# Performance work log

Hardware: AMD Instinct MI355X
Metric: run time of the kernel (lower is better)

Reference implementation:

```python
import jax, jax.numpy as jnp
import numpy as np

BS, SEQ, D_MODEL, N_HEADS = 4, 2048, 1024, 16
D_HEAD = D_MODEL // N_HEADS


def setup_inputs() -> dict:
    key = jax.random.key(0)
    ks = jax.random.split(key, 12)
    s = 1.0 / np.sqrt(D_MODEL)
    return {
        "Q": jax.random.normal(ks[0], (BS, SEQ, D_MODEL), jnp.float32),
        "K": jax.random.normal(ks[1], (BS, SEQ, D_MODEL), jnp.float32),
        "V": jax.random.normal(ks[2], (BS, SEQ, D_MODEL), jnp.float32),
        "mask": jax.random.randint(ks[3], (BS, 1, 1, SEQ), 0, 2, jnp.int32),
        "Wq": jax.random.normal(ks[4], (D_MODEL, D_MODEL), jnp.float32) * s,
        "bq": jnp.zeros((D_MODEL,), jnp.float32),
        "Wk": jax.random.normal(ks[5], (D_MODEL, D_MODEL), jnp.float32) * s,
        "bk": jnp.zeros((D_MODEL,), jnp.float32),
        "Wv": jax.random.normal(ks[6], (D_MODEL, D_MODEL), jnp.float32) * s,
        "bv": jnp.zeros((D_MODEL,), jnp.float32),
        "Wo": jax.random.normal(ks[7], (D_MODEL, D_MODEL), jnp.float32) * s,
        "bo": jnp.zeros((D_MODEL,), jnp.float32),
    }


def _split_heads(x):
    # (b, s, d_model) -> (b, h, s, d_head)
    b, s, _ = x.shape
    return x.reshape(b, s, N_HEADS, D_HEAD).transpose(0, 2, 1, 3)


def reference(Q, K, V, mask, Wq, bq, Wk, bk, Wv, bv, Wo, bo):
    q = _split_heads(Q @ Wq.T + bq)
    k = _split_heads(K @ Wk.T + bk)
    v = _split_heads(V @ Wv.T + bv)
    # (b, h, sq, sk) score matrix, scaled by sqrt(d_head)
    scores = jnp.einsum("bhqd,bhkd->bhqk", q, k) / np.sqrt(D_HEAD).astype(np.float32)
    scores = jnp.where(mask == 0, jnp.float32(-1e9), scores)
    attn = jax.nn.softmax(scores, axis=-1)
    ctx = jnp.einsum("bhqk,bhkd->bhqd", attn, v)
    b, h, s, d = ctx.shape
    ctx = ctx.transpose(0, 2, 1, 3).reshape(b, s, h * d)
    return ctx @ Wo.T + bo
```

## Files before the change

kernel.cpp:

```cpp
#include <hip/hip_runtime.h>


typedef __attribute__((ext_vector_type(8))) unsigned short us8;
typedef __attribute__((ext_vector_type(4))) unsigned short us4;
typedef __attribute__((ext_vector_type(4))) int i4;
typedef __attribute__((ext_vector_type(4))) float f4;
typedef __attribute__((ext_vector_type(4))) float f32x4;
typedef __attribute__((ext_vector_type(8))) __bf16 bf16x8;
typedef __attribute__((ext_vector_type(2))) unsigned u32x2;
typedef __attribute__((ext_vector_type(4))) unsigned u32x4;

#define DEV static __device__ __forceinline__

DEV unsigned short f2bf(float f){
  unsigned u = __builtin_bit_cast(unsigned, f);
  u = (u + 0x7fffu + ((u >> 16) & 1u)) >> 16;
  return (unsigned short)u;
}

DEV bf16x8 ld_frag(const unsigned short* p){
  return __builtin_bit_cast(bf16x8, *(const us8*)p);
}

DEV void gll16(const unsigned short* gsrc, unsigned short* ldst){
  __builtin_amdgcn_global_load_lds(
      (const __attribute__((address_space(1))) unsigned int*)gsrc,
      (__attribute__((address_space(3))) unsigned int*)ldst, 16, 0, 0);
}

DEV us8 ld_cvt_f32x8(const float* p){
  f4 v0 = *(const f4*)p;
  f4 v1 = *(const f4*)(p + 4);
  unsigned d0, d1, d2, d3;
  asm("v_cvt_pk_bf16_f32 %0, %1, %2" : "=v"(d0) : "v"(v0[0]), "v"(v0[1]));
  asm("v_cvt_pk_bf16_f32 %0, %1, %2" : "=v"(d1) : "v"(v0[2]), "v"(v0[3]));
  asm("v_cvt_pk_bf16_f32 %0, %1, %2" : "=v"(d2) : "v"(v1[0]), "v"(v1[1]));
  asm("v_cvt_pk_bf16_f32 %0, %1, %2" : "=v"(d3) : "v"(v1[2]), "v"(v1[3]));
  u32x4 u = {d0, d1, d2, d3};
  return __builtin_bit_cast(us8, u);
}

__global__ __launch_bounds__(256) void mask_scan(
    const int* __restrict__ mask, int* __restrict__ idx, int* __restrict__ nk)
{
  const int b = blockIdx.x, t = threadIdx.x;
  __shared__ int sc[256];
  int m[8]; int c = 0;
#pragma unroll
  for(int r = 0; r < 8; ++r){ m[r] = mask[b * 2048 + t * 8 + r]; c += (m[r] != 0); }
  sc[t] = c;
  __syncthreads();
  for(int s = 1; s < 256; s <<= 1){
    int v = (t >= s) ? sc[t - s] : 0;
    __syncthreads();
    sc[t] += v;
    __syncthreads();
  }
  int pos = sc[t] - c;
  int total = sc[255];
#pragma unroll
  for(int r = 0; r < 8; ++r) if(m[r]) idx[b * 2048 + pos++] = t * 8 + r;
  int pend = (total + 127) & ~127;
  for(int p = total + t; p < pend; p += 256) idx[b * 2048 + p] = 0;
  if(t == 0) nk[b] = total;
}

__global__ __launch_bounds__(256) void cvt_all(
    const float* __restrict__ Wq, const float* __restrict__ Wk,
    const float* __restrict__ Wv, const float* __restrict__ Wo,
    const float* __restrict__ Qf, const float* __restrict__ Kf, const float* __restrict__ Vf,
    unsigned short* __restrict__ Wqb, unsigned short* __restrict__ Wkb,
    unsigned short* __restrict__ Wvb, unsigned short* __restrict__ Wob,
    unsigned short* __restrict__ Qb, unsigned short* __restrict__ Kbc,
    unsigned short* __restrict__ Vbc,
    const int* __restrict__ gidx, const int* __restrict__ nkarr)
{
  const int y = blockIdx.y, x = blockIdx.x, t = threadIdx.x;
  if(y < 4){
    if(x >= 512) return;
    const float* src = (y == 0) ? Wq : (y == 1) ? Wk : (y == 2) ? Wv : Wo;
    unsigned short* dst = (y == 0) ? Wqb : (y == 1) ? Wkb : (y == 2) ? Wvb : Wob;
    size_t i = (size_t)x * 2048 + t * 8;
    *(us8*)(dst + i) = ld_cvt_f32x8(src + i);
  } else if(y == 4){
    size_t i = (size_t)x * 2048 + t * 8;
    *(us8*)(Qb + i) = ld_cvt_f32x8(Qf + i);
  } else {
    const float* src = (y == 5) ? Kf : Vf;
    unsigned short* dst = (y == 5) ? Kbc : Vbc;
    int r0 = x * 2;
    int b = r0 >> 11, j = r0 & 2047;
    if(j >= ((nkarr[b] + 127) & ~127)) return;
    int rr = t >> 7;
    int srow = gidx[b * 2048 + j + rr];
    int col = (t & 127) * 8;
    *(us8*)(dst + (size_t)(r0 + rr) * 1024 + col) =
        ld_cvt_f32x8(src + ((size_t)b * 2048 + srow) * 1024 + col);
  }
}

__global__ __launch_bounds__(256) void qkv_proj(
    const unsigned short* __restrict__ Qb, const unsigned short* __restrict__ Kbc,
    const unsigned short* __restrict__ Vbc,
    const unsigned short* __restrict__ Wqb, const unsigned short* __restrict__ Wkb,
    const unsigned short* __restrict__ Wvb,
    const float* __restrict__ bq, const float* __restrict__ bk, const float* __restrict__ bv,
    unsigned short* __restrict__ qs, unsigned short* __restrict__ ksc,
    unsigned short* __restrict__ vTc, float qscale, const int* __restrict__ nkarr)
{
  __shared__ __align__(16) unsigned short As[2][128 * 64];
  __shared__ __align__(16) unsigned short Bs[2][128 * 64];
  const int tid = threadIdx.x;
  const int x = blockIdx.x, z = blockIdx.y >> 3, ny = blockIdx.y & 7;
  const int w = tid >> 6, l = tid & 63, g = l >> 4, l15 = l & 15;
  const int wm = w >> 1, wn = w & 1;
  const int xsw = ((l & 7) ^ (l >> 3)) << 3;

  if(z >= 1){
    const int gb = (x * 128) >> 11, j0 = (x * 128) & 2047;
    if(j0 >= ((nkarr[gb] + 127) & ~127)) return;
  }

  const unsigned short* Ab = (z == 0) ? Qb : (z == 1) ? Kbc : Wvb;
  const unsigned short* Bb = (z == 0) ? Wqb : (z == 1) ? Wkb : Vbc;
  const int abase = (z == 2) ? ny * 128 : x * 128;
  const int bbase = (z == 2) ? x * 128 : ny * 128;
  const int lrow = (w << 5) + (l >> 3);

  f32x4 acc[4][4];
#pragma unroll
  for(int a = 0; a < 4; ++a)
#pragma unroll
    for(int b = 0; b < 4; ++b) acc[a][b] = (f32x4){0.f,0.f,0.f,0.f};

  auto STAGE = [&](int kt, int nb){
#pragma unroll
    for(int j = 0; j < 4; ++j)
      gll16(Ab + (size_t)(abase + lrow + (j << 3)) * 1024 + kt * 64 + xsw,
            &As[nb][((w << 5) + (j << 3)) << 6]);
#pragma unroll
    for(int j = 0; j < 4; ++j)
      gll16(Bb + (size_t)(bbase + lrow + (j << 3)) * 1024 + kt * 64 + xsw,
            &Bs[nb][((w << 5) + (j << 3)) << 6]);
  };

  STAGE(0, 0);
  asm volatile("s_waitcnt vmcnt(0)" ::: "memory");
  __syncthreads();

  for(int kt = 0; kt < 16; ++kt){
    const int cur = kt & 1, nxt = cur ^ 1;
    if(kt + 1 < 16) STAGE(kt + 1, nxt);
#pragma unroll
    for(int kk = 0; kk < 2; ++kk){
      bf16x8 af[4], bg[4];
#pragma unroll
      for(int mi = 0; mi < 4; ++mi){
        int row = wm * 64 + mi * 16 + l15;
        af[mi] = ld_frag(&As[cur][row * 64 + ((kk * 32 + g * 8) ^ ((row & 7) << 3))]);
      }
#pragma unroll
      for(int ni = 0; ni < 4; ++ni){
        int row = wn * 64 + ni * 16 + l15;
        bg[ni] = ld_frag(&Bs[cur][row * 64 + ((kk * 32 + g * 8) ^ ((row & 7) << 3))]);
      }
#pragma unroll
      for(int mi = 0; mi < 4; ++mi)
#pragma unroll
        for(int ni = 0; ni < 4; ++ni)
          acc[mi][ni] = __builtin_amdgcn_mfma_f32_16x16x32_bf16(af[mi], bg[ni], acc[mi][ni], 0, 0, 0);
    }
    asm volatile("s_waitcnt vmcnt(0)" ::: "memory");
    __syncthreads();
  }

  if(z < 2){
    const float scale = (z == 0) ? qscale : 1.0f;
    const float* bias = (z == 0) ? bq : bk;
    unsigned short* out = (z == 0) ? qs : ksc;
#pragma unroll
    for(int mi = 0; mi < 4; ++mi)
#pragma unroll
      for(int ni = 0; ni < 4; ++ni){
        int gmb = x * 128 + wm * 64 + mi * 16 + g * 4;
        int gn  = ny * 128 + wn * 64 + ni * 16 + l15;
#pragma unroll
        for(int r = 0; r < 4; ++r){
          int gm = gmb + r;
          float v = (acc[mi][ni][r] + bias[gn]) * scale;
          int b = gm >> 11, s = gm & 2047, h = gn >> 6, dh = gn & 63;
          out[(size_t)(((b << 4) + h) * 2048 + s) * 64 + dh] = f2bf(v);
        }
      }
  } else {
#pragma unroll
    for(int mi = 0; mi < 4; ++mi)
#pragma unroll
      for(int ni = 0; ni < 4; ++ni){
        int gmb = ny * 128 + wm * 64 + mi * 16 + g * 4;
        int gn  = x * 128 + wn * 64 + ni * 16 + l15;
#pragma unroll
        for(int r = 0; r < 4; ++r){
          int gm = gmb + r;
          float v = acc[mi][ni][r] + bv[gm];
          int h = gm >> 6, dh = gm & 63, b = gn >> 11, s = gn & 2047;
          vTc[(size_t)(((b << 4) + h) * 64 + dh) * 2048 + s] = f2bf(v);
        }
      }
  }
}

__global__ __launch_bounds__(256) void gemm_out(
    const unsigned short* __restrict__ Ap, const unsigned short* __restrict__ Bp,
    const float* __restrict__ bias, float* __restrict__ outp, int K)
{
  __shared__ __align__(16) unsigned short As[2][128 * 64];
  __shared__ __align__(16) unsigned short Bs[2][128 * 64];
  const int tid = threadIdx.x;
  const int gy = blockIdx.x, gx = blockIdx.y;
  const int w = tid >> 6, l = tid & 63, g = l >> 4, l15 = l & 15;
  const int wm = w >> 1, wn = w & 1;
  const int xsw = ((l & 7) ^ (l >> 3)) << 3;
  const int lrow = (w << 5) + (l >> 3);

  f32x4 acc[4][4];
#pragma unroll
  for(int a = 0; a < 4; ++a)
#pragma unroll
    for(int b = 0; b < 4; ++b) acc[a][b] = (f32x4){0.f,0.f,0.f,0.f};

  auto STAGE = [&](int kt, int nb){
#pragma unroll
    for(int j = 0; j < 4; ++j)
      gll16(Ap + (size_t)(gy * 128 + lrow + (j << 3)) * K + kt * 64 + xsw,
            &As[nb][((w << 5) + (j << 3)) << 6]);
#pragma unroll
    for(int j = 0; j < 4; ++j)
      gll16(Bp + (size_t)(gx * 128 + lrow + (j << 3)) * K + kt * 64 + xsw,
            &Bs[nb][((w << 5) + (j << 3)) << 6]);
  };

  const int nkt = K >> 6;
  STAGE(0, 0);
  asm volatile("s_waitcnt vmcnt(0)" ::: "memory");
  __syncthreads();

  for(int kt = 0; kt < nkt; ++kt){
    const int cur = kt & 1, nxt = cur ^ 1;
    if(kt + 1 < nkt) STAGE(kt + 1, nxt);
#pragma unroll
    for(int kk = 0; kk < 2; ++kk){
      bf16x8 af[4], bg[4];
#pragma unroll
      for(int mi = 0; mi < 4; ++mi){
        int row = wm * 64 + mi * 16 + l15;
        af[mi] = ld_frag(&As[cur][row * 64 + ((kk * 32 + g * 8) ^ ((row & 7) << 3))]);
      }
#pragma unroll
      for(int ni = 0; ni < 4; ++ni){
        int row = wn * 64 + ni * 16 + l15;
        bg[ni] = ld_frag(&Bs[cur][row * 64 + ((kk * 32 + g * 8) ^ ((row & 7) << 3))]);
      }
#pragma unroll
      for(int mi = 0; mi < 4; ++mi)
#pragma unroll
        for(int ni = 0; ni < 4; ++ni)
          acc[mi][ni] = __builtin_amdgcn_mfma_f32_16x16x32_bf16(af[mi], bg[ni], acc[mi][ni], 0, 0, 0);
    }
    asm volatile("s_waitcnt vmcnt(0)" ::: "memory");
    __syncthreads();
  }

#pragma unroll
  for(int mi = 0; mi < 4; ++mi)
#pragma unroll
    for(int ni = 0; ni < 4; ++ni){
      int gmb = gy * 128 + wm * 64 + mi * 16 + g * 4;
      int gn  = gx * 128 + wn * 64 + ni * 16 + l15;
#pragma unroll
      for(int r = 0; r < 4; ++r)
        outp[(size_t)(gmb + r) * 1024 + gn] = acc[mi][ni][r] + bias[gn];
    }
}

__global__ __launch_bounds__(256) void attn_kernel(
    const unsigned short* __restrict__ q, const unsigned short* __restrict__ ksc,
    const unsigned short* __restrict__ vTc, const int* __restrict__ nk,
    unsigned short* __restrict__ ctx)
{
  __shared__ __align__(16) unsigned short KsB[2][64 * 64];
  __shared__ __align__(16) unsigned short VtB[2][64 * 64];
  __shared__ __align__(16) unsigned short Ps[4][16 * 64];

  const int bh = blockIdx.x;
  const int qt = blockIdx.y;
  const int b  = bh >> 4, h = bh & 15;
  const int tid = threadIdx.x;
  const int w = tid >> 6, l = tid & 63, g = l >> 4, l15 = l & 15;
  const int rl = l >> 3, c8 = l & 7;

  const int nkb = nk[b];
  const int nt = (nkb + 63) >> 6;

  const unsigned short* qbase = q + ((size_t)(bh * 2048 + qt * 64 + w * 16 + l15)) * 64;
  bf16x8 bq[2];
  bq[0] = ld_frag(qbase + g * 8);
  bq[1] = ld_frag(qbase + 32 + g * 8);

  const unsigned short* kbase = ksc + (size_t)bh * 2048 * 64;
  const unsigned short* vbase = vTc + (size_t)bh * 64 * 2048;

  const unsigned short* kg0 = kbase + (size_t)(w * 16 + rl) * 64 + c8 * 8;
  const unsigned short* vg0 = vbase + (size_t)(w * 16 + rl) * 2048 + c8 * 8;
  const int lo0 = (w * 16 + rl) * 64 + ((c8 ^ rl) << 3);
  const int lo1 = lo0 + 8 * 64;

  us8 kr0, kr1, vr0, vr1;
#define LOAD_T(kt_) do{                                        \
    kr0 = *(const us8*)(kg0 + (size_t)(kt_) * 4096);           \
    kr1 = *(const us8*)(kg0 + (size_t)(kt_) * 4096 + 512);     \
    vr0 = *(const us8*)(vg0 + (size_t)(kt_) * 64);             \
    vr1 = *(const us8*)(vg0 + (size_t)(kt_) * 64 + 8 * 2048);  \
  }while(0)
#define WRITE_T(bb_) do{                                       \
    *(us8*)&KsB[bb_][lo0] = kr0;                               \
    *(us8*)&KsB[bb_][lo1] = kr1;                               \
    *(us8*)&VtB[bb_][lo0] = vr0;                               \
    *(us8*)&VtB[bb_][lo1] = vr1;                               \
  }while(0)

  f32x4 acc[4];
#pragma unroll
  for(int mi = 0; mi < 4; ++mi) acc[mi] = (f32x4){0.f,0.f,0.f,0.f};
  float ll = 0.f;

  LOAD_T(0);
  WRITE_T(0);
  __syncthreads();

  for(int kt = 0; kt < nt; ++kt){
    const int bb = kt & 1;
    if(kt + 1 < nt) LOAD_T(kt + 1);

    f32x4 sa[4];
#pragma unroll
    for(int mi = 0; mi < 4; ++mi) sa[mi] = (f32x4){0.f,0.f,0.f,0.f};
    __builtin_amdgcn_s_setprio(1);
#pragma unroll
    for(int kk = 0; kk < 2; ++kk){
#pragma unroll
      for(int mi = 0; mi < 4; ++mi){
        int row = mi * 16 + l15;
        bf16x8 af = ld_frag(&KsB[bb][row * 64 + ((kk * 32 + g * 8) ^ ((row & 7) << 3))]);
        sa[mi] = __builtin_amdgcn_mfma_f32_16x16x32_bf16(af, bq[kk], sa[mi], 0, 0, 0);
      }
    }
    __builtin_amdgcn_s_setprio(0);

    float p[4][4];
    if((kt + 1) * 64 <= nkb){
#pragma unroll
      for(int mi = 0; mi < 4; ++mi)
#pragma unroll
        for(int r = 0; r < 4; ++r){
          p[mi][r] = __builtin_amdgcn_exp2f(sa[mi][r]);
          ll += p[mi][r];
        }
    } else {
      int kb0 = kt * 64 + g * 4;
#pragma unroll
      for(int mi = 0; mi < 4; ++mi)
#pragma unroll
        for(int r = 0; r < 4; ++r){
          float e = __builtin_amdgcn_exp2f(sa[mi][r]);
          p[mi][r] = (kb0 + mi * 16 + r < nkb) ? e : 0.f;
          ll += p[mi][r];
        }
    }

#pragma unroll
    for(int mi = 0; mi < 4; ++mi){
      unsigned d0, d1;
      asm("v_cvt_pk_bf16_f32 %0, %1, %2" : "=v"(d0) : "v"(p[mi][0]), "v"(p[mi][1]));
      asm("v_cvt_pk_bf16_f32 %0, %1, %2" : "=v"(d1) : "v"(p[mi][2]), "v"(p[mi][3]));
      u32x2 dd = {d0, d1};
      *(u32x2*)&Ps[w][l15 * 64 + ((mi * 16 + g * 4) ^ ((l15 & 7) << 3))] = dd;
    }

    __builtin_amdgcn_s_setprio(1);
#pragma unroll
    for(int kk = 0; kk < 2; ++kk){
      bf16x8 pb = ld_frag(&Ps[w][l15 * 64 + ((kk * 32 + g * 8) ^ ((l15 & 7) << 3))]);
#pragma unroll
      for(int mi = 0; mi < 4; ++mi){
        int row = mi * 16 + l15;
        bf16x8 av = ld_frag(&VtB[bb][row * 64 + ((kk * 32 + g * 8) ^ ((row & 7) << 3))]);
        acc[mi] = __builtin_amdgcn_mfma_f32_16x16x32_bf16(av, pb, acc[mi], 0, 0, 0);
      }
    }
    __builtin_amdgcn_s_setprio(0);

    if(kt + 1 < nt) WRITE_T(bb ^ 1);
    __syncthreads();
  }

  ll += __shfl_xor(ll, 16);
  ll += __shfl_xor(ll, 32);
  float inv = 1.0f / ll;

  {
    int qrow = w * 16 + l15;
#pragma unroll
    for(int mi = 0; mi < 4; ++mi){
      us4 o;
#pragma unroll
      for(int r = 0; r < 4; ++r) o[r] = f2bf(acc[mi][r] * inv);
      *(us4*)&KsB[0][qrow * 64 + ((mi * 16 + g * 4) ^ ((qrow & 7) << 3))] = o;
    }
  }
  __syncthreads();
  {
    int qrow = tid >> 2, part = tid & 3;
    us8 v0 = *(const us8*)&KsB[0][qrow * 64 + ((part * 16)     ^ ((qrow & 7) << 3))];
    us8 v1 = *(const us8*)&KsB[0][qrow * 64 + ((part * 16 + 8) ^ ((qrow & 7) << 3))];
    size_t orow = ((size_t)b * 2048 + qt * 64 + qrow) * 1024 + h * 64 + part * 16;
    *(us8*)&ctx[orow] = v0;
    *(us8*)&ctx[orow + 8] = v1;
  }
#undef LOAD_T
#undef WRITE_T
}

extern "C" void kernel_launch(void* const* d_in, const int* in_sizes, int n_in,
                              void* d_out, int out_size, void* d_ws, size_t ws_size,
                              hipStream_t stream) {
  const float* Qf = (const float*)d_in[0];
  const float* Kf = (const float*)d_in[1];
  const float* Vf = (const float*)d_in[2];
  const int*   Mk = (const int*)d_in[3];
  const float* Wq = (const float*)d_in[4];
  const float* bq = (const float*)d_in[5];
  const float* Wk = (const float*)d_in[6];
  const float* bk = (const float*)d_in[7];
  const float* Wv = (const float*)d_in[8];
  const float* bv = (const float*)d_in[9];
  const float* Wo = (const float*)d_in[10];
  const float* bo = (const float*)d_in[11];

  const size_t MB = 1u << 20;
  char* ws = (char*)d_ws;
  unsigned short* Wqb = (unsigned short*)(ws + 0 * MB);
  unsigned short* Wkb = (unsigned short*)(ws + 2 * MB);
  unsigned short* Wvb = (unsigned short*)(ws + 4 * MB);
  unsigned short* Wob = (unsigned short*)(ws + 6 * MB);
  unsigned short* qs  = (unsigned short*)(ws + 8 * MB);
  unsigned short* ksc = (unsigned short*)(ws + 24 * MB);
  unsigned short* vTc = (unsigned short*)(ws + 40 * MB);
  unsigned short* ctx = (unsigned short*)(ws + 56 * MB);
  int* idx = (int*)(ws + 72 * MB);
  int* nk  = (int*)(ws + 73 * MB);
  unsigned short* Qb  = (unsigned short*)(ws + 74 * MB);
  unsigned short* Kbc = (unsigned short*)(ws + 90 * MB);
  unsigned short* Vbc = (unsigned short*)(ws + 106 * MB);

  mask_scan<<<4, 256, 0, stream>>>(Mk, idx, nk);
  cvt_all<<<dim3(4096, 7), 256, 0, stream>>>(Wq, Wk, Wv, Wo, Qf, Kf, Vf,
                                             Wqb, Wkb, Wvb, Wob, Qb, Kbc, Vbc,
                                             idx, nk);

  const float QSCALE = 0.125f * 1.4426950408889634f;
  dim3 blk(256);
  qkv_proj<<<dim3(64, 24), blk, 0, stream>>>(Qb, Kbc, Vbc, Wqb, Wkb, Wvb,
                                             bq, bk, bv, qs, ksc, vTc, QSCALE, nk);
  attn_kernel<<<dim3(64, 32), blk, 0, stream>>>(qs, ksc, vTc, nk, ctx);
  gemm_out<<<dim3(64, 8), blk, 0, stream>>>(ctx, Wob, bo, (float*)d_out, 1024);
}
```

Baseline: 173.3 us.

## Widen QKV projection tile to 128x256 and compute transposed W·X

The QKV projection now computes W·Xᵀ for all three projections with a 256-wide weight tile and a 128-row activation tile per block, halving the grid. The transposed orientation lets the Q and K epilogues write four contiguous bf16 values per store and load bias as a float4. The double-buffered LDS pipeline is replaced by a single buffer with a sync before and after each load, which removes load/compute overlap. Accumulator registers double to 32 fragments, which may lower occupancy.

New measurement: 201.8 us. +16.4%, slower.

```diff
diff --git a/kernel.cpp b/kernel.cpp
--- a/kernel.cpp
+++ b/kernel.cpp
@@ -108,70 +108,58 @@
     unsigned short* __restrict__ qs, unsigned short* __restrict__ ksc,
     unsigned short* __restrict__ vTc, float qscale, const int* __restrict__ nkarr)
 {
-  __shared__ __align__(16) unsigned short As[2][128 * 64];
-  __shared__ __align__(16) unsigned short Bs[2][128 * 64];
+  __shared__ __align__(16) unsigned short Ws[256 * 64];
+  __shared__ __align__(16) unsigned short Xs[128 * 64];
   const int tid = threadIdx.x;
-  const int x = blockIdx.x, z = blockIdx.y >> 3, ny = blockIdx.y & 7;
+  const int x = blockIdx.x, z = blockIdx.y >> 2, ny = blockIdx.y & 3;
   const int w = tid >> 6, l = tid & 63, g = l >> 4, l15 = l & 15;
   const int wm = w >> 1, wn = w & 1;
   const int xsw = ((l & 7) ^ (l >> 3)) << 3;
+  const int rl8 = l >> 3;
 
   if(z >= 1){
     const int gb = (x * 128) >> 11, j0 = (x * 128) & 2047;
     if(j0 >= ((nkarr[gb] + 127) & ~127)) return;
   }
 
-  const unsigned short* Ab = (z == 0) ? Qb : (z == 1) ? Kbc : Wvb;
-  const unsigned short* Bb = (z == 0) ? Wqb : (z == 1) ? Wkb : Vbc;
-  const int abase = (z == 2) ? ny * 128 : x * 128;
-  const int bbase = (z == 2) ? x * 128 : ny * 128;
-  const int lrow = (w << 5) + (l >> 3);
-
-  f32x4 acc[4][4];
-#pragma unroll
-  for(int a = 0; a < 4; ++a)
+  const unsigned short* Xb = (z == 0) ? Qb : (z == 1) ? Kbc : Vbc;
+  const unsigned short* Wb = (z == 0) ? Wqb : (z == 1) ? Wkb : Wvb;
+
+  f32x4 acc[8][4];
+#pragma unroll
+  for(int a = 0; a < 8; ++a)
 #pragma unroll
     for(int b = 0; b < 4; ++b) acc[a][b] = (f32x4){0.f,0.f,0.f,0.f};
 
-  auto STAGE = [&](int kt, int nb){
+  for(int kt = 0; kt < 16; ++kt){
+    __syncthreads();
 #pragma unroll
     for(int j = 0; j < 4; ++j)
-      gll16(Ab + (size_t)(abase + lrow + (j << 3)) * 1024 + kt * 64 + xsw,
-            &As[nb][((w << 5) + (j << 3)) << 6]);
-#pragma unroll
-    for(int j = 0; j < 4; ++j)
-      gll16(Bb + (size_t)(bbase + lrow + (j << 3)) * 1024 + kt * 64 + xsw,
-            &Bs[nb][((w << 5) + (j << 3)) << 6]);
-  };
-
-  STAGE(0, 0);
-  asm volatile("s_waitcnt vmcnt(0)" ::: "memory");
-  __syncthreads();
-
-  for(int kt = 0; kt < 16; ++kt){
-    const int cur = kt & 1, nxt = cur ^ 1;
-    if(kt + 1 < 16) STAGE(kt + 1, nxt);
+      gll16(Xb + (size_t)(x * 128 + (w << 5) + (j << 3) + rl8) * 1024 + kt * 64 + xsw,
+            &Xs[((w << 5) + (j << 3)) << 6]);
+#pragma unroll
+    for(int j = 0; j < 8; ++j)
+      gll16(Wb + (size_t)(ny * 256 + (w << 6) + (j << 3) + rl8) * 1024 + kt * 64 + xsw,
+            &Ws[((w << 6) + (j << 3)) << 6]);
+    asm volatile("s_waitcnt vmcnt(0)" ::: "memory");
+    __syncthreads();
 #pragma unroll
     for(int kk = 0; kk < 2; ++kk){
-      bf16x8 af[4], bg[4];
-#pragma unroll
-      for(int mi = 0; mi < 4; ++mi){
-        int row = wm * 64 + mi * 16 + l15;
-        af[mi] = ld_frag(&As[cur][row * 64 + ((kk * 32 + g * 8) ^ ((row & 7) << 3))]);
-      }
-#pragma unroll
-      for(int ni = 0; ni < 4; ++ni){
-        int row = wn * 64 + ni * 16 + l15;
-        bg[ni] = ld_frag(&Bs[cur][row * 64 + ((kk * 32 + g * 8) ^ ((row & 7) << 3))]);
-      }
-#pragma unroll
-      for(int mi = 0; mi < 4; ++mi)
-#pragma unroll
-        for(int ni = 0; ni < 4; ++ni)
-          acc[mi][ni] = __builtin_amdgcn_mfma_f32_16x16x32_bf16(af[mi], bg[ni], acc[mi][ni], 0, 0, 0);
-    }
-    asm volatile("s_waitcnt vmcnt(0)" ::: "memory");
-    __syncthreads();
+      bf16x8 bg[4];
+#pragma unroll
+      for(int ai = 0; ai < 4; ++ai){
+        int row = wm * 64 + ai * 16 + l15;
+        bg[ai] = ld_frag(&Xs[row * 64 + ((kk * 32 + g * 8) ^ ((row & 7) << 3))]);
+      }
+#pragma unroll
+      for(int wi = 0; wi < 8; ++wi){
+        int row = wn * 128 + wi * 16 + l15;
+        bf16x8 af = ld_frag(&Ws[row * 64 + ((kk * 32 + g * 8) ^ ((row & 7) << 3))]);
+#pragma unroll
+        for(int ai = 0; ai < 4; ++ai)
+          acc[wi][ai] = __builtin_amdgcn_mfma_f32_16x16x32_bf16(af, bg[ai], acc[wi][ai], 0, 0, 0);
+      }
+    }
   }
 
   if(z < 2){
@@ -179,34 +167,37 @@
     const float* bias = (z == 0) ? bq : bk;
     unsigned short* out = (z == 0) ? qs : ksc;
 #pragma unroll
-    for(int mi = 0; mi < 4; ++mi)
-#pragma unroll
-      for(int ni = 0; ni < 4; ++ni){
-        int gmb = x * 128 + wm * 64 + mi * 16 + g * 4;
-        int gn  = ny * 128 + wn * 64 + ni * 16 + l15;
+    for(int wi = 0; wi < 8; ++wi){
+      int gnb = ny * 256 + wn * 128 + wi * 16 + g * 4;
+      f4 bb = *(const f4*)&bias[gnb];
+      int h = gnb >> 6, dh = gnb & 63;
+#pragma unroll
+      for(int ai = 0; ai < 4; ++ai){
+        int gm = x * 128 + wm * 64 + ai * 16 + l15;
+        int b = gm >> 11, s = gm & 2047;
+        us4 o;
+#pragma unroll
+        for(int r = 0; r < 4; ++r) o[r] = f2bf((acc[wi][ai][r] + bb[r]) * scale);
+        *(us4*)&out[(size_t)(((b << 4) + h) * 2048 + s) * 64 + dh] = o;
+      }
+    }
+  } else {
+#pragma unroll
+    for(int wi = 0; wi < 8; ++wi){
+      int gdb = ny * 256 + wn * 128 + wi * 16 + g * 4;
+      f4 bb = *(const f4*)&bv[gdb];
+#pragma unroll
+      for(int ai = 0; ai < 4; ++ai){
+        int gn = x * 128 + wm * 64 + ai * 16 + l15;
+        int b = gn >> 11, s = gn & 2047;
 #pragma unroll
         for(int r = 0; r < 4; ++r){
-          int gm = gmb + r;
-          float v = (acc[mi][ni][r] + bias[gn]) * scale;
-          int b = gm >> 11, s = gm & 2047, h = gn >> 6, dh = gn & 63;
-          out[(size_t)(((b << 4) + h) * 2048 + s) * 64 + dh] = f2bf(v);
+          int gd = gdb + r;
+          int h = gd >> 6, dh = gd & 63;
+          vTc[(size_t)(((b << 4) + h) * 64 + dh) * 2048 + s] = f2bf(acc[wi][ai][r] + bb[r]);
         }
       }
-  } else {
-#pragma unroll
-    for(int mi = 0; mi < 4; ++mi)
-#pragma unroll
-      for(int ni = 0; ni < 4; ++ni){
-        int gmb = ny * 128 + wm * 64 + mi * 16 + g * 4;
-        int gn  = x * 128 + wn * 64 + ni * 16 + l15;
-#pragma unroll
-        for(int r = 0; r < 4; ++r){
-          int gm = gmb + r;
-          float v = acc[mi][ni][r] + bv[gm];
-          int h = gm >> 6, dh = gm & 63, b = gn >> 11, s = gn & 2047;
-          vTc[(size_t)(((b << 4) + h) * 64 + dh) * 2048 + s] = f2bf(v);
-        }
-      }
+    }
   }
 }
 
@@ -470,7 +461,7 @@
 
   const float QSCALE = 0.125f * 1.4426950408889634f;
   dim3 blk(256);
-  qkv_proj<<<dim3(64, 24), blk, 0, stream>>>(Qb, Kbc, Vbc, Wqb, Wkb, Wvb,
+  qkv_proj<<<dim3(64, 12), blk, 0, stream>>>(Qb, Kbc, Vbc, Wqb, Wkb, Wvb,
                                              bq, bk, bv, qs, ksc, vTc, QSCALE, nk);
   attn_kernel<<<dim3(64, 32), blk, 0, stream>>>(qs, ksc, vTc, nk, ctx);
   gemm_out<<<dim3(64, 8), blk, 0, stream>>>(ctx, Wob, bo, (float*)d_out, 1024);
```

## Prefetch two k-tiles ahead with partial vmcnt waits in projection GEMMs

Applied to the files above, without the earlier changes.

Restructures the double-buffered GEMM main loops in the QKV and output projection kernels. Tiles 0 and 1 are now issued before the loop. Each iteration waits only until the older tile's 8 loads have landed (vmcnt(8)) instead of draining all outstanding loads. After compute and a barrier, the next-next tile is loaded into the freed buffer. This keeps one tile of global-to-LDS loads in flight during MFMA work to hide memory latency, at the cost of relying on exact vmcnt counting and explicit sched_barriers.

Result: faster. 165.1 us (-4.7%).

```diff
diff --git a/kernel.cpp b/kernel.cpp
--- a/kernel.cpp
+++ b/kernel.cpp
@@ -145,12 +145,15 @@
   };
 
   STAGE(0, 0);
-  asm volatile("s_waitcnt vmcnt(0)" ::: "memory");
-  __syncthreads();
+  STAGE(1, 1);
 
   for(int kt = 0; kt < 16; ++kt){
-    const int cur = kt & 1, nxt = cur ^ 1;
-    if(kt + 1 < 16) STAGE(kt + 1, nxt);
+    const int cur = kt & 1;
+    if(kt + 1 < 16) asm volatile("s_waitcnt vmcnt(8)" ::: "memory");
+    else            asm volatile("s_waitcnt vmcnt(0)" ::: "memory");
+    __builtin_amdgcn_sched_barrier(0);
+    __builtin_amdgcn_s_barrier();
+    __builtin_amdgcn_sched_barrier(0);
 #pragma unroll
     for(int kk = 0; kk < 2; ++kk){
       bf16x8 af[4], bg[4];
@@ -170,8 +173,10 @@
         for(int ni = 0; ni < 4; ++ni)
           acc[mi][ni] = __builtin_amdgcn_mfma_f32_16x16x32_bf16(af[mi], bg[ni], acc[mi][ni], 0, 0, 0);
     }
-    asm volatile("s_waitcnt vmcnt(0)" ::: "memory");
-    __syncthreads();
+    __builtin_amdgcn_sched_barrier(0);
+    __builtin_amdgcn_s_barrier();
+    __builtin_amdgcn_sched_barrier(0);
+    if(kt + 2 < 16) STAGE(kt + 2, cur);
   }
 
   if(z < 2){
@@ -242,12 +247,15 @@
 
   const int nkt = K >> 6;
   STAGE(0, 0);
-  asm volatile("s_waitcnt vmcnt(0)" ::: "memory");
-  __syncthreads();
+  STAGE(1, 1);
 
   for(int kt = 0; kt < nkt; ++kt){
-    const int cur = kt & 1, nxt = cur ^ 1;
-    if(kt + 1 < nkt) STAGE(kt + 1, nxt);
+    const int cur = kt & 1;
+    if(kt + 1 < nkt) asm volatile("s_waitcnt vmcnt(8)" ::: "memory");
+    else             asm volatile("s_waitcnt vmcnt(0)" ::: "memory");
+    __builtin_amdgcn_sched_barrier(0);
+    __builtin_amdgcn_s_barrier();
+    __builtin_amdgcn_sched_barrier(0);
 #pragma unroll
     for(int kk = 0; kk < 2; ++kk){
       bf16x8 af[4], bg[4];
@@ -267,8 +275,10 @@
         for(int ni = 0; ni < 4; ++ni)
           acc[mi][ni] = __builtin_amdgcn_mfma_f32_16x16x32_bf16(af[mi], bg[ni], acc[mi][ni], 0, 0, 0);
     }
-    asm volatile("s_waitcnt vmcnt(0)" ::: "memory");
-    __syncthreads();
+    __builtin_amdgcn_sched_barrier(0);
+    __builtin_amdgcn_s_barrier();
+    __builtin_amdgcn_sched_barrier(0);
+    if(kt + 2 < nkt) STAGE(kt + 2, cur);
   }
 
 #pragma unroll
```
